# Kernel tuning notes

Measured on AMD Instinct MI355X. Metric: run time of the kernel, lower is better.

The kernel has to match this reference:

```python
import jax, jax.numpy as jnp
import numpy as np

H = 128      # hidden_sizes
E = 128      # embedding_size
V = 100000   # n_words
C = 10       # n_classes
B, S, L = 32, 32, 64
PAD = 0


def _gru_dir(x, w_ih, w_hh, b_ih, b_hh, reverse):
    # x: [N, T, D]; torch GRU cell convention (r, z, n gate order)
    xp = jnp.einsum('ntd,gd->ntg', x, w_ih) + b_ih  # [N, T, 3H]
    if reverse:
        xp = xp[:, ::-1]
    h0 = jnp.zeros((x.shape[0], w_hh.shape[1]), x.dtype)

    def step(h, xt):
        gh = h @ w_hh.T + b_hh
        xr, xz, xn = jnp.split(xt, 3, axis=-1)
        hr, hz, hn = jnp.split(gh, 3, axis=-1)
        r = jax.nn.sigmoid(xr + hr)
        z = jax.nn.sigmoid(xz + hz)
        n = jnp.tanh(xn + r * hn)
        h2 = (1.0 - z) * n + z * h
        return h2, h2

    _, hs = jax.lax.scan(step, h0, jnp.swapaxes(xp, 0, 1))
    hs = jnp.swapaxes(hs, 0, 1)  # [N, T, H]
    if reverse:
        hs = hs[:, ::-1]
    return hs


def _bi_gru(x, pf, pb):
    return jnp.concatenate([_gru_dir(x, *pf, False), _gru_dir(x, *pb, True)], axis=-1)


def _attn_pool(h, W, b, ctx):
    # h: [N, T, 2H] -> pooled [N, 2H]
    u = jnp.tanh(jnp.einsum('ntd,ed->nte', h, W) + b)
    a = jax.nn.softmax(u @ ctx, axis=1)          # [N, T]
    return jnp.einsum('ntd,nt->nd', h, a)


def setup_inputs() -> dict:
    key = jax.random.key(0)
    ks = jax.random.split(key, 24)
    sc = 0.05
    d = {}
    d['X'] = jax.random.randint(ks[0], (B, S, L), 0, V, dtype=jnp.int32)
    d['emb'] = jax.random.normal(ks[1], (V, E), jnp.float32) * sc
    # word-level bi-GRU (input E)
    d['w_ih_f'] = jax.random.normal(ks[2], (3 * H, E), jnp.float32) * sc
    d['w_hh_f'] = jax.random.normal(ks[3], (3 * H, H), jnp.float32) * sc
    d['b_ih_f'] = jnp.zeros((3 * H,), jnp.float32)
    d['b_hh_f'] = jnp.zeros((3 * H,), jnp.float32)
    d['w_ih_b'] = jax.random.normal(ks[4], (3 * H, E), jnp.float32) * sc
    d['w_hh_b'] = jax.random.normal(ks[5], (3 * H, H), jnp.float32) * sc
    d['b_ih_b'] = jnp.zeros((3 * H,), jnp.float32)
    d['b_hh_b'] = jnp.zeros((3 * H,), jnp.float32)
    d['Ww'] = jax.random.normal(ks[6], (2 * H, 2 * H), jnp.float32) * sc
    d['bw'] = jnp.zeros((2 * H,), jnp.float32)
    d['ctx_w'] = jax.random.normal(ks[7], (2 * H,), jnp.float32) * sc
    # sentence-level bi-GRU (input 2H)
    d['s_ih_f'] = jax.random.normal(ks[8], (3 * H, 2 * H), jnp.float32) * sc
    d['s_hh_f'] = jax.random.normal(ks[9], (3 * H, H), jnp.float32) * sc
    d['sb_ih_f'] = jnp.zeros((3 * H,), jnp.float32)
    d['sb_hh_f'] = jnp.zeros((3 * H,), jnp.float32)
    d['s_ih_b'] = jax.random.normal(ks[10], (3 * H, 2 * H), jnp.float32) * sc
    d['s_hh_b'] = jax.random.normal(ks[11], (3 * H, H), jnp.float32) * sc
    d['sb_ih_b'] = jnp.zeros((3 * H,), jnp.float32)
    d['sb_hh_b'] = jnp.zeros((3 * H,), jnp.float32)
    d['Ws'] = jax.random.normal(ks[12], (2 * H, 2 * H), jnp.float32) * sc
    d['bs'] = jnp.zeros((2 * H,), jnp.float32)
    d['ctx_s'] = jax.random.normal(ks[13], (2 * H,), jnp.float32) * sc
    d['Wc'] = jax.random.normal(ks[14], (C, 2 * H), jnp.float32) * sc
    d['bc'] = jnp.zeros((C,), jnp.float32)
    return d


def reference(X, emb, w_ih_f, w_hh_f, b_ih_f, b_hh_f, w_ih_b, w_hh_b, b_ih_b, b_hh_b,
              Ww, bw, ctx_w, s_ih_f, s_hh_f, sb_ih_f, sb_hh_f, s_ih_b, s_hh_b,
              sb_ih_b, sb_hh_b, Ws, bs, ctx_s, Wc, bc):
    emb = emb.at[PAD].set(0.0)               # padding_idx semantics
    words = emb[X.reshape(B * S, L)]          # [B*S, L, E]
    h_w = _bi_gru(words, (w_ih_f, w_hh_f, b_ih_f, b_hh_f),
                  (w_ih_b, w_hh_b, b_ih_b, b_hh_b))  # [B*S, L, 2H]
    sents = _attn_pool(h_w, Ww, bw, ctx_w).reshape(B, S, 2 * H)
    h_s = _bi_gru(sents, (s_ih_f, s_hh_f, sb_ih_f, sb_hh_f),
                  (s_ih_b, s_hh_b, sb_ih_b, sb_hh_b))  # [B, S, 2H]
    doc = _attn_pool(h_s, Ws, bs, ctx_s)      # [B, 2H]
    return doc @ Wc.T + bc                    # [B, C]
```

## Files before the change

### kernel.cpp

```cpp
#include <hip/hip_runtime.h>
#include <hip/hip_bf16.h>
#include <math.h>

#define Bd 32
#define Sd 32
#define Ld 64
#define Ed 128
#define Hd 128
#define MW 65536
#define MS 1024

#define OFF_WIHT_S   0
#define OFF_WFW_W    196608
#define OFF_WFW_S    262144
#define OFF_W6       327680
#define OFF_BIH_W    622592
#define OFF_BIH_S    623360
#define OFF_BHH_W    624128
#define OFF_BHH_S    624896
#define OFF_WFX      625664
#define OFF_HW       723968
#define OFF_SENTS    17763328
#define OFF_XP_S     18025472
#define OFF_HS       18811904
#define OFF_DOC      19078144
#define OFF_WFHH     19086336
#define WS_FLOATS    19184640

typedef __attribute__((ext_vector_type(8))) short sh8;
typedef __attribute__((ext_vector_type(4))) float f32x4;
typedef unsigned short u16;
typedef unsigned int u32;

#define GLD  388
#define XPLD 385
#define HPLD 520

__device__ __forceinline__ float sigmoidf_(float x) {
    return __fdividef(1.0f, 1.0f + __expf(-x));
}
__device__ __forceinline__ float tanhf_(float x) {
    float t = __expf(-2.0f * fabsf(x));
    float r = __fdividef(1.0f - t, 1.0f + t);
    return copysignf(r, x);
}
__device__ __forceinline__ u16 bf16_hi(float f) {
    u32 x = __float_as_uint(f);
    return (u16)((x + 0x7fffu + ((x >> 16) & 1u)) >> 16);
}
__device__ __forceinline__ float bf16_f(u16 u) { return __uint_as_float(((u32)u) << 16); }
__device__ __forceinline__ void bf16_split(float f, u16& hi, u16& lo) {
    hi = bf16_hi(f);
    lo = bf16_hi(f - bf16_f(hi));
}

__global__ void prep(const float* __restrict__ s_ih_f, const float* __restrict__ s_ih_b,
                     const float* __restrict__ w_ih_f, const float* __restrict__ w_ih_b,
                     const float* __restrict__ w_hh_f, const float* __restrict__ w_hh_b,
                     const float* __restrict__ s_hh_f, const float* __restrict__ s_hh_b,
                     const float* __restrict__ b_ih_f, const float* __restrict__ b_ih_b,
                     const float* __restrict__ sb_ih_f, const float* __restrict__ sb_ih_b,
                     const float* __restrict__ b_hh_f, const float* __restrict__ b_hh_b,
                     const float* __restrict__ sb_hh_f, const float* __restrict__ sb_hh_b,
                     float* __restrict__ ws)
{
    int i = blockIdx.x * 256 + threadIdx.x;
    if (i < 196608) {
        int k = i / 768, g = i % 768;
        ws[OFF_WIHT_S + i] = (g < 384) ? s_ih_f[g*256 + k] : s_ih_b[(g-384)*256 + k];
        return;
    }
    i -= 196608;
    if (i < 131072) return;
    i -= 131072;
    if (i < 294912) {
        int set = i / 49152, rem = i % 49152;
        int k4 = rem / 1536, r2 = rem % 1536, g = r2 >> 2, sub = r2 & 3;
        const float* w = (set==0) ? w_ih_f : (set==1) ? w_ih_b : (set==2) ? w_hh_f
                       : (set==3) ? w_hh_b : (set==4) ? s_hh_f : s_hh_b;
        ws[OFF_W6 + i] = w[g*128 + k4*4 + sub];
        return;
    }
    i -= 294912;
    if (i < 768) { ws[OFF_BIH_W + i] = (i<384) ? b_ih_f[i] : b_ih_b[i-384]; return; }
    i -= 768;
    if (i < 768) { ws[OFF_BIH_S + i] = (i<384) ? sb_ih_f[i] : sb_ih_b[i-384]; return; }
    i -= 768;
    if (i < 768) { ws[OFF_BHH_W + i] = (i<384) ? b_hh_f[i] : b_hh_b[i-384]; return; }
    i -= 768;
    if (i < 768) { ws[OFF_BHH_S + i] = (i<384) ? sb_hh_f[i] : sb_hh_b[i-384]; return; }
}

__global__ void prep2(const float* __restrict__ w_hh_f, const float* __restrict__ w_hh_b,
                      u16* __restrict__ WFo)
{
    int i = blockIdx.x * 256 + threadIdx.x;
    int within = i % 49152;
    int combo  = i / 49152;
    int half = combo & 1, dir = combo >> 1;
    int nt  = within / 2048;
    int r2  = within % 2048;
    int q   = r2 >> 9;
    int r3  = r2 & 511;
    int l   = r3 >> 3, e = r3 & 7;
    int n = nt*16 + (l & 15);
    int k = q*32 + ((l >> 4) << 3) + e;
    const float* src = dir ? w_hh_b : w_hh_f;
    float v = src[n*128 + k];
    u16 hi = bf16_hi(v);
    WFo[i] = half ? bf16_hi(v - bf16_f(hi)) : hi;
}

__global__ void prep3(const float* __restrict__ Ww, const float* __restrict__ Ws,
                      const float* __restrict__ w_ih_f, const float* __restrict__ w_ih_b,
                      u16* __restrict__ WFW_W, u16* __restrict__ WFW_S,
                      u16* __restrict__ WFX)
{
    int i = blockIdx.x * 256 + threadIdx.x;
    if (i < 262144) {
        int which = i / 131072;
        int w = i % 131072;
        int half = w / 65536;
        int r = w % 65536;
        int nt = r / 4096;
        int r2 = r % 4096;
        int q = r2 / 512;
        int l = (r2 % 512) >> 3, e = r2 & 7;
        int n = nt*16 + (l & 15);
        int k = q*32 + ((l >> 4) << 3) + e;
        const float* src = which ? Ws : Ww;
        float v = src[n*256 + k];
        u16 hi = bf16_hi(v);
        u16 o = half ? bf16_hi(v - bf16_f(hi)) : hi;
        (which ? WFW_S : WFW_W)[w] = o;
        return;
    }
    i -= 262144;
    if (i < 196608) {
        int w = i % 98304;
        int dir = i / 98304;
        int half = w / 49152;
        int r = w % 49152;
        int nt = r / 2048;
        int r2 = r % 2048;
        int q = r2 / 512;
        int l = (r2 % 512) >> 3, e = r2 & 7;
        int n = nt*16 + (l & 15);
        int k = q*32 + ((l >> 4) << 3) + e;
        const float* src = dir ? w_ih_b : w_ih_f;
        float v = src[n*128 + k];
        u16 hi = bf16_hi(v);
        WFX[i] = half ? bf16_hi(v - bf16_f(hi)) : hi;
        return;
    }
}

__global__ __launch_bounds__(768)
void gru_word_full(const int* __restrict__ X, const float* __restrict__ emb,
                   const u16* __restrict__ WFX, const u16* __restrict__ WFHH,
                   const float* __restrict__ b_ih_f, const float* __restrict__ b_ih_b,
                   const float* __restrict__ b_hh_f, const float* __restrict__ b_hh_b,
                   u16* __restrict__ houtp)
{
    const int bx = blockIdx.x;
    const int dir = bx >> 7;
    const int blk = bx & 127;
    const int seq0 = blk * 8;
    const int tid = threadIdx.x;
    const int lane = tid & 63;
    const int wid = tid >> 6;

    __shared__ float xp_lds[64 * XPLD];
    __shared__ f32x4 uni4[2048];
    __shared__ u16 h_pk[4 * HPLD];
    __shared__ int ids_s[8][64];
    float* G = (float*)uni4;
    u16* a_pk = (u16*)uni4;

    const int j = tid & 127;
    const int sg = tid >> 7;
    const bool gthread = tid < 512;
    const float* bih = dir ? b_ih_b : b_ih_f;
    const float* bhh = dir ? b_hh_b : b_hh_f;
    float bhr = 0.f, bhz = 0.f, bhn = 0.f;
    if (gthread) { bhr = bhh[j]; bhz = bhh[128 + j]; bhn = bhh[256 + j]; }

    const u16* WXbase = WFX + (long)dir * 98304;
    const u16* WHbase = WFHH + (long)dir * 98304;
    const int nt0 = wid*2, nt1 = wid*2 + 1;
    const int c0 = nt0*16 + (lane & 15);
    const int c1 = nt1*16 + (lane & 15);
    const int qj = j >> 5, subkj = (j >> 3) & 3, ej = j & 7;

    for (int i = tid; i < 512; i += 768)
        ids_s[i >> 6][i & 63] = X[(long)(seq0 + (i >> 6))*64 + (i & 63)];
    for (int i = tid; i < 4*HPLD; i += 768) h_pk[i] = 0;
    __syncthreads();

    float hprev0 = 0.f, hprev1 = 0.f;
    for (int c = 0; c < 8; ++c) {
        asm volatile("" ::: "memory");
        sh8 xh0[4], xl0[4], xh1[4], xl1[4];
#pragma unroll
        for (int q = 0; q < 4; ++q) {
            xh0[q] = *(const sh8*)(WXbase + (nt0*4 + q)*512 + lane*8);
            xl0[q] = *(const sh8*)(WXbase + 49152 + (nt0*4 + q)*512 + lane*8);
            xh1[q] = *(const sh8*)(WXbase + (nt1*4 + q)*512 + lane*8);
            xl1[q] = *(const sh8*)(WXbase + 49152 + (nt1*4 + q)*512 + lane*8);
        }
        const float bv0 = bih[c0], bv1 = bih[c1];
        for (int idx = tid; idx < 4096; idx += 768) {
            int cc = idx & 3, rm = (idx >> 2) & 7, subk = (idx >> 5) & 3;
            int q = (idx >> 7) & 3, mfs = idx >> 9;
            int ts = c*8 + rm;
            int t = dir ? 63 - ts : ts;
            int kk = q*32 + subk*8 + cc*2;
            int id = ids_s[mfs][t];
            float2 v = make_float2(0.f, 0.f);
            if (id != 0) v = *(const float2*)&emb[(long)id*128 + kk];
            u16 h0,l0,h1,l1; bf16_split(v.x,h0,l0); bf16_split(v.y,h1,l1);
            int lh = subk*16 + rm;
            *(u32*)&a_pk[(mfs*4 + q)*512 + lh*8 + cc*2]       = (u32)h0 | ((u32)h1 << 16);
            *(u32*)&a_pk[(mfs*4 + q)*512 + (lh+8)*8 + cc*2]   = (u32)l0 | ((u32)l1 << 16);
        }
        __syncthreads();
#pragma unroll
        for (int mf = 0; mf < 8; ++mf) {
            f32x4 A0 = (f32x4){0.f,0.f,0.f,0.f};
            f32x4 A1 = (f32x4){0.f,0.f,0.f,0.f};
#pragma unroll
            for (int q = 0; q < 4; ++q) {
                sh8 a = *(const sh8*)&a_pk[(mf*4 + q)*512 + lane*8];
                A0 = __builtin_amdgcn_mfma_f32_16x16x32_bf16(a, xh0[q], A0, 0,0,0);
                A0 = __builtin_amdgcn_mfma_f32_16x16x32_bf16(a, xl0[q], A0, 0,0,0);
                A1 = __builtin_amdgcn_mfma_f32_16x16x32_bf16(a, xh1[q], A1, 0,0,0);
                A1 = __builtin_amdgcn_mfma_f32_16x16x32_bf16(a, xl1[q], A1, 0,0,0);
            }
            float g0[4], g1[4];
#pragma unroll
            for (int r = 0; r < 4; ++r) {
                g0[r] = A0[r] + __shfl_xor(A0[r], 32);
                g1[r] = A1[r] + __shfl_xor(A1[r], 32);
            }
            if ((lane >= 32) == (mf & 1)) {
                int row = mf*8 + ((lane >> 4) & 1)*4;
#pragma unroll
                for (int r = 0; r < 4; ++r) {
                    xp_lds[(row+r)*XPLD + c0] = g0[r] + bv0;
                    xp_lds[(row+r)*XPLD + c1] = g1[r] + bv1;
                }
            }
        }
        __syncthreads();
        asm volatile("" ::: "memory");
        sh8 wh0[4], wl0[4], wh1[4], wl1[4];
#pragma unroll
        for (int q = 0; q < 4; ++q) {
            wh0[q] = *(const sh8*)(WHbase + (nt0*4 + q)*512 + lane*8);
            wl0[q] = *(const sh8*)(WHbase + 49152 + (nt0*4 + q)*512 + lane*8);
            wh1[q] = *(const sh8*)(WHbase + (nt1*4 + q)*512 + lane*8);
            wl1[q] = *(const sh8*)(WHbase + 49152 + (nt1*4 + q)*512 + lane*8);
        }
        for (int tt = 0; tt < 8; ++tt) {
            const int ts = c*8 + tt;
            const int t = dir ? 63 - ts : ts;
            f32x4 acc0 = (f32x4){0.f,0.f,0.f,0.f};
            f32x4 acc1 = (f32x4){0.f,0.f,0.f,0.f};
#pragma unroll
            for (int q = 0; q < 4; ++q) {
                sh8 hp = *(const sh8*)&h_pk[q*HPLD + lane*8];
                acc0 = __builtin_amdgcn_mfma_f32_16x16x32_bf16(hp, wh0[q], acc0, 0,0,0);
                acc0 = __builtin_amdgcn_mfma_f32_16x16x32_bf16(hp, wl0[q], acc0, 0,0,0);
                acc1 = __builtin_amdgcn_mfma_f32_16x16x32_bf16(hp, wh1[q], acc1, 0,0,0);
                acc1 = __builtin_amdgcn_mfma_f32_16x16x32_bf16(hp, wl1[q], acc1, 0,0,0);
            }
            {
                const int col16 = lane & 15;
                const int row0  = (lane >> 4) << 2;
#pragma unroll
                for (int r = 0; r < 4; ++r) {
                    G[(row0+r)*GLD + nt0*16 + col16] = acc0[r];
                    G[(row0+r)*GLD + nt1*16 + col16] = acc1[r];
                }
            }
            __syncthreads();
            if (gthread) {
#pragma unroll
                for (int si = 0; si < 2; ++si) {
                    const int s = sg + si*4;
                    float gr  = G[s*GLD + j]       + G[(s+8)*GLD + j]       + bhr;
                    float gz  = G[s*GLD + 128 + j] + G[(s+8)*GLD + 128 + j] + bhz;
                    float gnh = G[s*GLD + 256 + j] + G[(s+8)*GLD + 256 + j] + bhn;
                    const float* xrow = &xp_lds[(s*8 + tt)*XPLD];
                    float r  = sigmoidf_(xrow[j] + gr);
                    float z  = sigmoidf_(xrow[128 + j] + gz);
                    float nv = tanhf_(xrow[256 + j] + r * gnh);
                    float hold = si ? hprev1 : hprev0;
                    float hnew = (1.f - z) * nv + z * hold;
                    if (si) hprev1 = hnew; else hprev0 = hnew;
                    u16 hh, hl; bf16_split(hnew, hh, hl);
                    u16 ohh = (u16)__shfl_xor((int)hh, 1);
                    u16 ohl = (u16)__shfl_xor((int)hl, 1);
                    if ((j & 1) == 0) {
                        u32 w = (u32)hh | ((u32)ohh << 16);
                        *(u32*)&h_pk[qj*HPLD + (subkj*16 + s)*8 + ej] = w;
                    } else {
                        u32 w = (u32)ohl | ((u32)hl << 16);
                        *(u32*)&h_pk[qj*HPLD + (subkj*16 + s + 8)*8 + (ej - 1)] = w;
                    }
                    long b = ((long)(seq0+s)*64 + t)*512 + dir*128 + j;
                    houtp[b] = hh;
                    houtp[b + 256] = hl;
                }
            }
            __syncthreads();
        }
    }
}

template<int T, bool PACKED>
__global__ __launch_bounds__(1024)
void attn_fused(const float* __restrict__ A, const u16* __restrict__ WF,
                const float* __restrict__ bias, const float* __restrict__ ctx,
                float* __restrict__ outp)
{
    __shared__ u16 a_pk[8][8][512];
    __shared__ float pscore[8][8][17];
    __shared__ float aw[64];
    __shared__ float red[4][256];
    const int tid = threadIdx.x;
    const int lane = tid & 63;
    const int wid = tid >> 6;
    const int m0 = blockIdx.x * 64;

    sh8 bh[8], bl[8];
#pragma unroll
    for (int q = 0; q < 8; ++q) {
        bh[q] = *(const sh8*)(WF + (wid*8 + q)*512 + lane*8);
        bl[q] = *(const sh8*)(WF + 65536 + (wid*8 + q)*512 + lane*8);
    }
    const int colg = wid*16 + (lane & 15);
    const float bwv = bias[colg];
    const float cxv = ctx[colg];

    if (PACKED) {
        const u32* src32 = (const u32*)A + (long)blockIdx.x * 16384;
        u32* dst = (u32*)a_pk;
        for (int idx = tid; idx < 16384; idx += 1024) {
            int mf = idx >> 11, q = (idx >> 8) & 7, l = (idx >> 2) & 63, c2 = idx & 3;
            int row16 = l & 15, hilo = row16 >> 3, rm = row16 & 7;
            int t = mf*8 + rm;
            int k = q*32 + (l >> 4)*8 + c2*2;
            dst[idx] = src32[(t*2 + hilo)*128 + (k >> 1)];
        }
    } else {
        for (int idx = tid; idx < 8192; idx += 1024) {
            int row = idx >> 7;
            int k   = (idx & 127) << 1;
            float2 v = *(const float2*)&A[(long)(m0 + row)*256 + k];
            u16 h0,l0,h1,l1; bf16_split(v.x,h0,l0); bf16_split(v.y,h1,l1);
            int mf = row >> 3, rm = row & 7;
            int q = k >> 5;
            int lh = (((k & 31) >> 3) << 4) | rm;
            int e = k & 7;
            *(u32*)&a_pk[mf][q][lh*8 + e]     = (u32)h0 | ((u32)h1 << 16);
            *(u32*)&a_pk[mf][q][(lh+8)*8 + e] = (u32)l0 | ((u32)l1 << 16);
        }
    }
    __syncthreads();

#pragma unroll
    for (int mf = 0; mf < 8; ++mf) {
        f32x4 acc = (f32x4){0.f,0.f,0.f,0.f};
#pragma unroll
        for (int q = 0; q < 8; ++q) {
            sh8 a = *(const sh8*)&a_pk[mf][q][lane*8];
            acc = __builtin_amdgcn_mfma_f32_16x16x32_bf16(a, bh[q], acc, 0,0,0);
            acc = __builtin_amdgcn_mfma_f32_16x16x32_bf16(a, bl[q], acc, 0,0,0);
        }
        float g[4];
#pragma unroll
        for (int r = 0; r < 4; ++r) g[r] = acc[r] + __shfl_xor(acc[r], 32);
        if ((lane >= 32) == (mf & 1)) {
            float p[4];
#pragma unroll
            for (int r = 0; r < 4; ++r) p[r] = tanhf_(g[r] + bwv) * cxv;
#pragma unroll
            for (int r = 0; r < 4; ++r) {
                p[r] += __shfl_xor(p[r], 1);
                p[r] += __shfl_xor(p[r], 2);
                p[r] += __shfl_xor(p[r], 4);
                p[r] += __shfl_xor(p[r], 8);
            }
            if ((lane & 15) == 0) {
#pragma unroll
                for (int r = 0; r < 4; ++r)
                    pscore[mf][((lane >> 4) & 1)*4 + r][wid] = p[r];
            }
        }
    }
    __syncthreads();

    if (tid < 64) {
        float sc = 0.f;
#pragma unroll
        for (int w = 0; w < 16; ++w) sc += pscore[tid >> 3][tid & 7][w];
        float mx = sc;
#pragma unroll
        for (int m = 1; m < T; m <<= 1) mx = fmaxf(mx, __shfl_xor(mx, m));
        float e = __expf(sc - mx);
        float den = e;
#pragma unroll
        for (int m = 1; m < T; m <<= 1) den += __shfl_xor(den, m);
        aw[tid] = __fdividef(e, den);
    }
    __syncthreads();

    if (tid < 512) {
        const int dp = (tid & 127) << 1;
        const int tg = tid >> 7;
        const int q = dp >> 5, lhb = ((dp & 31) >> 3) << 4, e = dp & 7;
        float acc0 = 0.f, acc1 = 0.f;
#pragma unroll
        for (int i = 0; i < 16; ++i) {
            int t = tg*16 + i;
            int mf = t >> 3, rm = t & 7;
            const u16* base = &a_pk[mf][q][(lhb | rm)*8 + e];
            u32 hh = *(const u32*)base;
            u32 ll = *(const u32*)(base + 64);
            float h0 = bf16_f((u16)hh) + bf16_f((u16)ll);
            float h1 = bf16_f((u16)(hh >> 16)) + bf16_f((u16)(ll >> 16));
            float w = aw[t];
            acc0 = fmaf(w, h0, acc0);
            acc1 = fmaf(w, h1, acc1);
        }
        red[tg][dp] = acc0; red[tg][dp + 1] = acc1;
    }
    __syncthreads();
    if (T == 64) {
        if (tid < 256)
            outp[(long)blockIdx.x*256 + tid] = red[0][tid] + red[1][tid] + red[2][tid] + red[3][tid];
    } else {
        if (tid < 512) {
            int sent = tid >> 8, dd = tid & 255;
            outp[((long)blockIdx.x*2 + sent)*256 + dd] = red[sent*2][dd] + red[sent*2 + 1][dd];
        }
    }
}

__global__ __launch_bounds__(256)
void gemm_xp(const float* __restrict__ A,
             const float* __restrict__ WT, const float* __restrict__ bias,
             float* __restrict__ out, int N, int K)
{
    __shared__ float As[64*128];
    __shared__ float Bs[128*64];
    const int tid = threadIdx.x;
    const int m0 = blockIdx.x * 64;
    const int n0 = blockIdx.y * 64;
    const int tx = tid & 15, ty = tid >> 4;
    float acc[4][4];
#pragma unroll
    for (int i=0;i<4;i++)
#pragma unroll
        for (int c=0;c<4;c++) acc[i][c]=0.f;

    for (int kc = 0; kc < K; kc += 128) {
        if (kc) __syncthreads();
#pragma unroll
        for (int it = 0; it < 8; ++it) {
            int idx = tid + it*256;
            int r = idx >> 5, c4 = idx & 31;
            float4 v = *(const float4*)&A[(long)(m0 + r)*K + kc + (c4<<2)];
            *(float4*)&As[r*128 + ((c4 ^ (r & 7)) << 2)] = v;
        }
#pragma unroll
        for (int it = 0; it < 8; ++it) {
            int idx = tid + it*256;
            int k = idx >> 4, c4 = idx & 15;
            float4 v = *(const float4*)&WT[(long)(kc + k)*N + n0 + (c4<<2)];
            *(float4*)&Bs[k*64 + ((c4 ^ (k & 7)) << 2)] = v;
        }
        __syncthreads();
        const int swzA = (ty & 7) << 2;
#pragma unroll 4
        for (int k = 0; k < 128; ++k) {
            float4 b = *(const float4*)&Bs[k*64 + ((tx ^ (k & 7)) << 2)];
            int kx = k ^ swzA;
#pragma unroll
            for (int i=0;i<4;i++) {
                float a = As[(ty + 16*i)*128 + kx];
                acc[i][0] = fmaf(a, b.x, acc[i][0]);
                acc[i][1] = fmaf(a, b.y, acc[i][1]);
                acc[i][2] = fmaf(a, b.z, acc[i][2]);
                acc[i][3] = fmaf(a, b.w, acc[i][3]);
            }
        }
    }
    float4 bia = *(const float4*)&bias[n0 + (tx<<2)];
#pragma unroll
    for (int i=0;i<4;i++) {
        float4 res = make_float4(acc[i][0]+bia.x, acc[i][1]+bia.y, acc[i][2]+bia.z, acc[i][3]+bia.w);
        *(float4*)&out[(long)(m0 + ty + 16*i)*N + n0 + (tx<<2)] = res;
    }
}

template<int NSEQ, int T>
__global__ __launch_bounds__(512)
void gru_fused(const float* __restrict__ xp, const float4* __restrict__ whh4,
               const float* __restrict__ bhh, float* __restrict__ hout,
               int blocks_per_dir)
{
    const int bx = blockIdx.x;
    const int dir = bx / blocks_per_dir;
    const int blk = bx % blocks_per_dir;
    const int seq0 = blk * NSEQ;
    const int tid = threadIdx.x;
    const int kq = tid & 3;
    const int j  = tid >> 2;
    const float4* W = whh4 + (long)dir * 12288;
    __shared__ float h_lds[NSEQ][128];
    for (int idx = tid; idx < NSEQ*128; idx += 512) ((float*)h_lds)[idx] = 0.f;
    const float bhr = bhh[dir*384 + j];
    const float bhz = bhh[dir*384 + 128 + j];
    const float bhn = bhh[dir*384 + 256 + j];
    __syncthreads();

    for (int ts = 0; ts < T; ++ts) {
        const int t = dir ? (T - 1 - ts) : ts;
        float a0[NSEQ], a1[NSEQ], a2[NSEQ];
#pragma unroll
        for (int s=0;s<NSEQ;s++){a0[s]=0.f;a1[s]=0.f;a2[s]=0.f;}
#pragma unroll
        for (int ii = 0; ii < 8; ++ii) {
            const int k4 = kq + (ii << 2);
            float4 w0 = W[k4*384 + j];
            float4 w1 = W[k4*384 + 128 + j];
            float4 w2 = W[k4*384 + 256 + j];
#pragma unroll
            for (int s=0;s<NSEQ;s++) {
                float4 h4 = *(const float4*)&h_lds[s][k4 << 2];
                a0[s] = fmaf(w0.x,h4.x, fmaf(w0.y,h4.y, fmaf(w0.z,h4.z, fmaf(w0.w,h4.w, a0[s]))));
                a1[s] = fmaf(w1.x,h4.x, fmaf(w1.y,h4.y, fmaf(w1.z,h4.z, fmaf(w1.w,h4.w, a1[s]))));
                a2[s] = fmaf(w2.x,h4.x, fmaf(w2.y,h4.y, fmaf(w2.z,h4.z, fmaf(w2.w,h4.w, a2[s]))));
            }
        }
#pragma unroll
        for (int s=0;s<NSEQ;s++) {
            a0[s] += __shfl_xor(a0[s], 1); a0[s] += __shfl_xor(a0[s], 2);
            a1[s] += __shfl_xor(a1[s], 1); a1[s] += __shfl_xor(a1[s], 2);
            a2[s] += __shfl_xor(a2[s], 1); a2[s] += __shfl_xor(a2[s], 2);
        }
        __syncthreads();
        if (kq == 0) {
#pragma unroll
            for (int s=0;s<NSEQ;s++) {
                const float* xr = &xp[((long)(seq0+s)*T + t)*768 + dir*384];
                float r = sigmoidf_(xr[j]       + a0[s] + bhr);
                float z = sigmoidf_(xr[128 + j] + a1[s] + bhz);
                float nv = tanhf_(xr[256 + j] + r * (a2[s] + bhn));
                float hold = h_lds[s][j];
                float hnew = (1.f - z) * nv + z * hold;
                h_lds[s][j] = hnew;
                hout[((long)(seq0+s)*T + t)*256 + dir*128 + j] = hnew;
            }
        }
        __syncthreads();
    }
}

__global__ void classifier(const float* __restrict__ doc, const float* __restrict__ Wc,
                           const float* __restrict__ bc, float* __restrict__ out)
{
    int tid = threadIdx.x;
    if (tid < 320) {
        int b = tid / 10, c = tid % 10;
        float s = bc[c];
        for (int d = 0; d < 256; ++d) s = fmaf(doc[b*256 + d], Wc[c*256 + d], s);
        out[tid] = s;
    }
}

extern "C" void kernel_launch(void* const* d_in, const int* in_sizes, int n_in,
                              void* d_out, int out_size, void* d_ws, size_t ws_size,
                              hipStream_t stream) {
    const int*   X       = (const int*)  d_in[0];
    const float* emb     = (const float*)d_in[1];
    const float* w_ih_f  = (const float*)d_in[2];
    const float* w_hh_f  = (const float*)d_in[3];
    const float* b_ih_f  = (const float*)d_in[4];
    const float* b_hh_f  = (const float*)d_in[5];
    const float* w_ih_b  = (const float*)d_in[6];
    const float* w_hh_b  = (const float*)d_in[7];
    const float* b_ih_b  = (const float*)d_in[8];
    const float* b_hh_b  = (const float*)d_in[9];
    const float* Ww      = (const float*)d_in[10];
    const float* bw      = (const float*)d_in[11];
    const float* ctx_w   = (const float*)d_in[12];
    const float* s_ih_f  = (const float*)d_in[13];
    const float* s_hh_f  = (const float*)d_in[14];
    const float* sb_ih_f = (const float*)d_in[15];
    const float* sb_hh_f = (const float*)d_in[16];
    const float* s_ih_b  = (const float*)d_in[17];
    const float* s_hh_b  = (const float*)d_in[18];
    const float* sb_ih_b = (const float*)d_in[19];
    const float* sb_hh_b = (const float*)d_in[20];
    const float* Ws      = (const float*)d_in[21];
    const float* bs      = (const float*)d_in[22];
    const float* ctx_s   = (const float*)d_in[23];
    const float* Wc      = (const float*)d_in[24];
    const float* bc      = (const float*)d_in[25];
    float* ws  = (float*)d_ws;
    float* out = (float*)d_out;

    if (ws_size < (size_t)WS_FLOATS * 4) return;

    prep<<<2444, 256, 0, stream>>>(s_ih_f, s_ih_b, w_ih_f, w_ih_b,
                                   w_hh_f, w_hh_b, s_hh_f, s_hh_b,
                                   b_ih_f, b_ih_b, sb_ih_f, sb_ih_b,
                                   b_hh_f, b_hh_b, sb_hh_f, sb_hh_b, ws);
    prep2<<<768, 256, 0, stream>>>(w_hh_f, w_hh_b, (u16*)(ws + OFF_WFHH));
    prep3<<<1792, 256, 0, stream>>>(Ww, Ws, w_ih_f, w_ih_b,
                                    (u16*)(ws + OFF_WFW_W), (u16*)(ws + OFF_WFW_S),
                                    (u16*)(ws + OFF_WFX));

    gru_word_full<<<256, 768, 0, stream>>>(
        X, emb, (const u16*)(ws + OFF_WFX), (const u16*)(ws + OFF_WFHH),
        b_ih_f, b_ih_b, b_hh_f, b_hh_b, (u16*)(ws + OFF_HW));

    attn_fused<64, true><<<1024, 1024, 0, stream>>>(
        ws + OFF_HW, (const u16*)(ws + OFF_WFW_W), bw, ctx_w, ws + OFF_SENTS);

    gemm_xp<<<dim3(16, 12), 256, 0, stream>>>(
        ws + OFF_SENTS, ws + OFF_WIHT_S, ws + OFF_BIH_S, ws + OFF_XP_S, 768, 256);
    gru_fused<1, 32><<<64, 512, 0, stream>>>(
        ws + OFF_XP_S, (const float4*)(ws + OFF_W6) + 4*12288, ws + OFF_BHH_S, ws + OFF_HS, 32);
    attn_fused<32, false><<<16, 1024, 0, stream>>>(
        ws + OFF_HS, (const u16*)(ws + OFF_WFW_S), bs, ctx_s, ws + OFF_DOC);
    classifier<<<1, 320, 0, stream>>>(ws + OFF_DOC, Wc, bc, out);
}
```

Baseline: 348.9 us.

## Overlap embedding staging with GRU recurrence and keep gate sums in registers

The recurrent step now has each of 8 waves compute the r, z and n gate tiles for one 16-column slice, so the gate nonlinearity runs directly from MFMA accumulators. This removes the shared-memory G buffer and one barrier per timestep. The 4 spare waves stage and bf16-split the next chunk's embedding rows into a dedicated LDS buffer while the recurrence runs, taking the gather off the critical path. Hidden-state global stores are buffered in registers and written after each 8-step chunk. The cost is higher register pressure, with 24 weight fragments held per wave, and idle MFMA capacity in the staging waves.

```diff
diff --git a/kernel.cpp b/kernel.cpp
--- a/kernel.cpp
+++ b/kernel.cpp
@@ -32,7 +32,6 @@
 typedef unsigned short u16;
 typedef unsigned int u32;
 
-#define GLD  388
 #define XPLD 385
 #define HPLD 520
 
@@ -155,6 +154,25 @@
     }
 }
 
+__device__ __forceinline__ void stage_emb(int idx, int c, int dir,
+                                          const float* __restrict__ emb,
+                                          const int (*ids_s)[64],
+                                          u16* __restrict__ a_pk)
+{
+    int cc = idx & 3, rm = (idx >> 2) & 7, subk = (idx >> 5) & 3;
+    int q = (idx >> 7) & 3, mfs = idx >> 9;
+    int ts = c*8 + rm;
+    int t = dir ? 63 - ts : ts;
+    int kk = q*32 + subk*8 + cc*2;
+    int id = ids_s[mfs][t];
+    float2 v = make_float2(0.f, 0.f);
+    if (id != 0) v = *(const float2*)&emb[(long)id*128 + kk];
+    u16 h0,l0,h1,l1; bf16_split(v.x,h0,l0); bf16_split(v.y,h1,l1);
+    int lh = subk*16 + rm;
+    *(u32*)&a_pk[(mfs*4 + q)*512 + lh*8 + cc*2]       = (u32)h0 | ((u32)h1 << 16);
+    *(u32*)&a_pk[(mfs*4 + q)*512 + (lh+8)*8 + cc*2]   = (u32)l0 | ((u32)l1 << 16);
+}
+
 __global__ __launch_bounds__(768)
 void gru_word_full(const int* __restrict__ X, const float* __restrict__ emb,
                    const u16* __restrict__ WFX, const u16* __restrict__ WFHH,
@@ -171,30 +189,36 @@
     const int wid = tid >> 6;
 
     __shared__ float xp_lds[64 * XPLD];
-    __shared__ f32x4 uni4[2048];
+    __shared__ u16 a_pk[8 * 4 * 512];
     __shared__ u16 h_pk[4 * HPLD];
     __shared__ int ids_s[8][64];
-    float* G = (float*)uni4;
-    u16* a_pk = (u16*)uni4;
-
-    const int j = tid & 127;
-    const int sg = tid >> 7;
-    const bool gthread = tid < 512;
+
     const float* bih = dir ? b_ih_b : b_ih_f;
     const float* bhh = dir ? b_hh_b : b_hh_f;
-    float bhr = 0.f, bhz = 0.f, bhn = 0.f;
-    if (gthread) { bhr = bhh[j]; bhz = bhh[128 + j]; bhn = bhh[256 + j]; }
 
     const u16* WXbase = WFX + (long)dir * 98304;
     const u16* WHbase = WFHH + (long)dir * 98304;
     const int nt0 = wid*2, nt1 = wid*2 + 1;
     const int c0 = nt0*16 + (lane & 15);
     const int c1 = nt1*16 + (lane & 15);
+
+    const int col16 = lane & 15;
+    const int j  = wid*16 + col16;
+    const int half = lane >> 5;
+    const int lq   = (lane >> 4) & 1;
+    const int sb   = lq*4 + half*2;
+    const int r0   = half*2;
     const int qj = j >> 5, subkj = (j >> 3) & 3, ej = j & 7;
+    float bhr = 0.f, bhz = 0.f, bhn = 0.f;
+    if (wid < 8) { bhr = bhh[j]; bhz = bhh[128 + j]; bhn = bhh[256 + j]; }
 
     for (int i = tid; i < 512; i += 768)
         ids_s[i >> 6][i & 63] = X[(long)(seq0 + (i >> 6))*64 + (i & 63)];
     for (int i = tid; i < 4*HPLD; i += 768) h_pk[i] = 0;
+    __syncthreads();
+
+    for (int idx = tid; idx < 4096; idx += 768)
+        stage_emb(idx, 0, dir, emb, ids_s, a_pk);
     __syncthreads();
 
     float hprev0 = 0.f, hprev1 = 0.f;
@@ -209,21 +233,6 @@
             xl1[q] = *(const sh8*)(WXbase + 49152 + (nt1*4 + q)*512 + lane*8);
         }
         const float bv0 = bih[c0], bv1 = bih[c1];
-        for (int idx = tid; idx < 4096; idx += 768) {
-            int cc = idx & 3, rm = (idx >> 2) & 7, subk = (idx >> 5) & 3;
-            int q = (idx >> 7) & 3, mfs = idx >> 9;
-            int ts = c*8 + rm;
-            int t = dir ? 63 - ts : ts;
-            int kk = q*32 + subk*8 + cc*2;
-            int id = ids_s[mfs][t];
-            float2 v = make_float2(0.f, 0.f);
-            if (id != 0) v = *(const float2*)&emb[(long)id*128 + kk];
-            u16 h0,l0,h1,l1; bf16_split(v.x,h0,l0); bf16_split(v.y,h1,l1);
-            int lh = subk*16 + rm;
-            *(u32*)&a_pk[(mfs*4 + q)*512 + lh*8 + cc*2]       = (u32)h0 | ((u32)h1 << 16);
-            *(u32*)&a_pk[(mfs*4 + q)*512 + (lh+8)*8 + cc*2]   = (u32)l0 | ((u32)l1 << 16);
-        }
-        __syncthreads();
 #pragma unroll
         for (int mf = 0; mf < 8; ++mf) {
             f32x4 A0 = (f32x4){0.f,0.f,0.f,0.f};
@@ -253,51 +262,58 @@
         }
         __syncthreads();
         asm volatile("" ::: "memory");
-        sh8 wh0[4], wl0[4], wh1[4], wl1[4];
-#pragma unroll
-        for (int q = 0; q < 4; ++q) {
-            wh0[q] = *(const sh8*)(WHbase + (nt0*4 + q)*512 + lane*8);
-            wl0[q] = *(const sh8*)(WHbase + 49152 + (nt0*4 + q)*512 + lane*8);
-            wh1[q] = *(const sh8*)(WHbase + (nt1*4 + q)*512 + lane*8);
-            wl1[q] = *(const sh8*)(WHbase + 49152 + (nt1*4 + q)*512 + lane*8);
-        }
+        sh8 wrh[4], wrl[4], wzh[4], wzl[4], wnh[4], wnl[4];
+        if (wid < 8) {
+#pragma unroll
+            for (int q = 0; q < 4; ++q) {
+                wrh[q] = *(const sh8*)(WHbase + ((wid     )*4 + q)*512 + lane*8);
+                wrl[q] = *(const sh8*)(WHbase + 49152 + ((wid     )*4 + q)*512 + lane*8);
+                wzh[q] = *(const sh8*)(WHbase + ((wid +  8)*4 + q)*512 + lane*8);
+                wzl[q] = *(const sh8*)(WHbase + 49152 + ((wid +  8)*4 + q)*512 + lane*8);
+                wnh[q] = *(const sh8*)(WHbase + ((wid + 16)*4 + q)*512 + lane*8);
+                wnl[q] = *(const sh8*)(WHbase + 49152 + ((wid + 16)*4 + q)*512 + lane*8);
+            }
+        }
+        u32 hpack0[8], hpack1[8];
+#pragma unroll
         for (int tt = 0; tt < 8; ++tt) {
-            const int ts = c*8 + tt;
-            const int t = dir ? 63 - ts : ts;
-            f32x4 acc0 = (f32x4){0.f,0.f,0.f,0.f};
-            f32x4 acc1 = (f32x4){0.f,0.f,0.f,0.f};
-#pragma unroll
-            for (int q = 0; q < 4; ++q) {
-                sh8 hp = *(const sh8*)&h_pk[q*HPLD + lane*8];
-                acc0 = __builtin_amdgcn_mfma_f32_16x16x32_bf16(hp, wh0[q], acc0, 0,0,0);
-                acc0 = __builtin_amdgcn_mfma_f32_16x16x32_bf16(hp, wl0[q], acc0, 0,0,0);
-                acc1 = __builtin_amdgcn_mfma_f32_16x16x32_bf16(hp, wh1[q], acc1, 0,0,0);
-                acc1 = __builtin_amdgcn_mfma_f32_16x16x32_bf16(hp, wl1[q], acc1, 0,0,0);
-            }
-            {
-                const int col16 = lane & 15;
-                const int row0  = (lane >> 4) << 2;
+            if (wid < 8) {
+                sh8 hp[4];
+#pragma unroll
+                for (int q = 0; q < 4; ++q) hp[q] = *(const sh8*)&h_pk[q*HPLD + lane*8];
+                f32x4 aR = (f32x4){0.f,0.f,0.f,0.f};
+                f32x4 aZ = (f32x4){0.f,0.f,0.f,0.f};
+                f32x4 aN = (f32x4){0.f,0.f,0.f,0.f};
+#pragma unroll
+                for (int q = 0; q < 4; ++q) {
+                    aR = __builtin_amdgcn_mfma_f32_16x16x32_bf16(hp[q], wrh[q], aR, 0,0,0);
+                    aR = __builtin_amdgcn_mfma_f32_16x16x32_bf16(hp[q], wrl[q], aR, 0,0,0);
+                    aZ = __builtin_amdgcn_mfma_f32_16x16x32_bf16(hp[q], wzh[q], aZ, 0,0,0);
+                    aZ = __builtin_amdgcn_mfma_f32_16x16x32_bf16(hp[q], wzl[q], aZ, 0,0,0);
+                    aN = __builtin_amdgcn_mfma_f32_16x16x32_bf16(hp[q], wnh[q], aN, 0,0,0);
+                    aN = __builtin_amdgcn_mfma_f32_16x16x32_bf16(hp[q], wnl[q], aN, 0,0,0);
+                }
+                float gR[4], gZ[4], gN[4];
 #pragma unroll
                 for (int r = 0; r < 4; ++r) {
-                    G[(row0+r)*GLD + nt0*16 + col16] = acc0[r];
-                    G[(row0+r)*GLD + nt1*16 + col16] = acc1[r];
+                    gR[r] = aR[r] + __shfl_xor(aR[r], 32);
+                    gZ[r] = aZ[r] + __shfl_xor(aZ[r], 32);
+                    gN[r] = aN[r] + __shfl_xor(aN[r], 32);
                 }
-            }
-            __syncthreads();
-            if (gthread) {
-#pragma unroll
-                for (int si = 0; si < 2; ++si) {
-                    const int s = sg + si*4;
-                    float gr  = G[s*GLD + j]       + G[(s+8)*GLD + j]       + bhr;
-                    float gz  = G[s*GLD + 128 + j] + G[(s+8)*GLD + 128 + j] + bhz;
-                    float gnh = G[s*GLD + 256 + j] + G[(s+8)*GLD + 256 + j] + bhn;
+#pragma unroll
+                for (int i = 0; i < 2; ++i) {
+                    const int s = sb + i;
+                    const int r = r0 + i;
+                    float grt = gR[r] + bhr;
+                    float gzt = gZ[r] + bhz;
+                    float gnt = gN[r] + bhn;
                     const float* xrow = &xp_lds[(s*8 + tt)*XPLD];
-                    float r  = sigmoidf_(xrow[j] + gr);
-                    float z  = sigmoidf_(xrow[128 + j] + gz);
-                    float nv = tanhf_(xrow[256 + j] + r * gnh);
-                    float hold = si ? hprev1 : hprev0;
-                    float hnew = (1.f - z) * nv + z * hold;
-                    if (si) hprev1 = hnew; else hprev0 = hnew;
+                    float rg = sigmoidf_(xrow[j] + grt);
+                    float zg = sigmoidf_(xrow[128 + j] + gzt);
+                    float nv = tanhf_(xrow[256 + j] + rg * gnt);
+                    float hold = i ? hprev1 : hprev0;
+                    float hnew = (1.f - zg) * nv + zg * hold;
+                    if (i) hprev1 = hnew; else hprev0 = hnew;
                     u16 hh, hl; bf16_split(hnew, hh, hl);
                     u16 ohh = (u16)__shfl_xor((int)hh, 1);
                     u16 ohl = (u16)__shfl_xor((int)hl, 1);
@@ -308,12 +324,28 @@
                         u32 w = (u32)ohl | ((u32)hl << 16);
                         *(u32*)&h_pk[qj*HPLD + (subkj*16 + s + 8)*8 + (ej - 1)] = w;
                     }
-                    long b = ((long)(seq0+s)*64 + t)*512 + dir*128 + j;
-                    houtp[b] = hh;
-                    houtp[b + 256] = hl;
+                    u32 pk = (u32)hh | ((u32)hl << 16);
+                    if (i) hpack1[tt] = pk; else hpack0[tt] = pk;
                 }
+            } else if (c < 7) {
+                const int st = tid - 512;
+                stage_emb(tt*512 + st,        c + 1, dir, emb, ids_s, a_pk);
+                stage_emb(tt*512 + 256 + st,  c + 1, dir, emb, ids_s, a_pk);
             }
             __syncthreads();
+        }
+        if (wid < 8) {
+#pragma unroll
+            for (int tt = 0; tt < 8; ++tt) {
+                const int ts = c*8 + tt;
+                const int t = dir ? 63 - ts : ts;
+                long b0 = ((long)(seq0 + sb)*64 + t)*512 + dir*128 + j;
+                long b1 = ((long)(seq0 + sb + 1)*64 + t)*512 + dir*128 + j;
+                houtp[b0]       = (u16)hpack0[tt];
+                houtp[b0 + 256] = (u16)(hpack0[tt] >> 16);
+                houtp[b1]       = (u16)hpack1[tt];
+                houtp[b1 + 256] = (u16)(hpack1[tt] >> 16);
+            }
         }
     }
 }
```

After: 590.3 us. +69.2%, slower.
